# Optimization experiments

Measured on AMD Instinct MI355X. Metric: run time of the kernel, lower is better.

The kernel has to match this reference:

```python
import jax, jax.numpy as jnp
import numpy as np

B, T, D, NH, L, E, K = 2, 1024, 512, 8, 4, 8, 2
H = D * 4
HD = D // NH
EPS = 1e-5
THETA = 10000.0
MOE_LAYERS = (0, 2)   # layer_idx % moe_freq == 0
DENSE_LAYERS = (1, 3)


def setup_inputs() -> dict:
    key = jax.random.key(0)
    ks = jax.random.split(key, 12)
    s = 0.02
    return {
        "x": jax.random.normal(ks[0], (B, T, D), jnp.float32),
        "qkv_w": jax.random.normal(ks[1], (L, 3 * D, D), jnp.float32) * s,
        "out_w": jax.random.normal(ks[2], (L, D, D), jnp.float32) * s,
        "norm1_w": jnp.ones((L, D), jnp.float32),
        "norm2_w": jnp.ones((L, D), jnp.float32),
        "router_w": jax.random.normal(ks[3], (2, E, D), jnp.float32) * s,
        "moe_w1": jax.random.normal(ks[4], (2, E, H, D), jnp.float32) * s,
        "moe_w2": jax.random.normal(ks[5], (2, E, D, H), jnp.float32) * s,
        "moe_w3": jax.random.normal(ks[6], (2, E, H, D), jnp.float32) * s,
        "f_w1": jax.random.normal(ks[7], (2, H, D), jnp.float32) * s,
        "f_w2": jax.random.normal(ks[8], (2, D, H), jnp.float32) * s,
        "f_w3": jax.random.normal(ks[9], (2, H, D), jnp.float32) * s,
        "norm_f": jnp.ones((D,), jnp.float32),
    }


def rmsnorm(x, w):
    return w * x * jax.lax.rsqrt(jnp.mean(x * x, axis=-1, keepdims=True) + EPS)


def rope_tables():
    inv_freq = 1.0 / (THETA ** (jnp.arange(0, HD, 2, dtype=jnp.float32) / HD))  # [HD/2]
    t = jnp.arange(T, dtype=jnp.float32)
    freqs = t[:, None] * inv_freq[None, :]  # [T, HD/2]
    return jnp.cos(freqs), jnp.sin(freqs)


def apply_rope(x, cos, sin):  # x: [B, NH, T, HD]
    x1, x2 = jnp.split(x, 2, axis=-1)
    return jnp.concatenate([x1 * cos - x2 * sin, x1 * sin + x2 * cos], axis=-1)


def attention(x, qkv_w, out_w, cos, sin, causal):
    qkv = x @ qkv_w.T  # [B, T, 3D]
    q, k, v = jnp.split(qkv, 3, axis=-1)
    sh = lambda a: a.reshape(B, T, NH, HD).transpose(0, 2, 1, 3)  # [B, NH, T, HD]
    q, k, v = sh(q), sh(k), sh(v)
    q = apply_rope(q, cos, sin)
    k = apply_rope(k, cos, sin)
    scores = jnp.einsum('bhqd,bhkd->bhqk', q, k) / np.sqrt(HD).astype(np.float32)
    scores = jnp.where(causal, scores, jnp.finfo(scores.dtype).min)
    attn = jax.nn.softmax(scores, axis=-1)
    out = jnp.einsum('bhqk,bhkd->bhqd', attn, v)
    out = out.transpose(0, 2, 1, 3).reshape(B, T, D)
    return out @ out_w.T


def swiglu(x, w1, w2, w3):
    return (jax.nn.silu(x @ w1.T) * (x @ w3.T)) @ w2.T


def moe(x, rw, w1, w2, w3):  # x: [N, D]
    n = x.shape[0]
    logits = x @ rw.T                              # [N, E]
    top_v, top_i = jax.lax.top_k(logits, K)        # [N, K]
    wts = jax.nn.softmax(top_v, axis=-1)           # [N, K]
    # combine[t, e] = sum_i wts[t, i] * 1[top_i[t, i] == e]
    combine = jnp.zeros((n, E), x.dtype).at[jnp.arange(n)[:, None], top_i].add(wts)
    gate = jax.nn.silu(jnp.einsum('nd,ehd->neh', x, w1))
    up = jnp.einsum('nd,ehd->neh', x, w3)
    expert_out = jnp.einsum('neh,edh->ned', gate * up, w2)  # [N, E, D]
    return jnp.einsum('ne,ned->nd', combine, expert_out)


def reference(x, qkv_w, out_w, norm1_w, norm2_w, router_w, moe_w1, moe_w2,
              moe_w3, f_w1, f_w2, f_w3, norm_f):
    cos, sin = rope_tables()
    causal = jnp.tril(jnp.ones((T, T), bool))
    h = x
    for l in range(L):
        h = h + attention(rmsnorm(h, norm1_w[l]), qkv_w[l], out_w[l], cos, sin, causal)
        hn = rmsnorm(h, norm2_w[l])
        if l in MOE_LAYERS:
            m = MOE_LAYERS.index(l)
            ff = moe(hn.reshape(-1, D), router_w[m], moe_w1[m], moe_w2[m], moe_w3[m]).reshape(B, T, D)
        else:
            m = DENSE_LAYERS.index(l)
            ff = swiglu(hn, f_w1[m], f_w2[m], f_w3[m])
        h = h + ff
    return rmsnorm(h, norm_f)
```

## Files before the change

kernel.cpp:

```cpp
#include <hip/hip_runtime.h>
#include <hip/hip_bf16.h>
#include <math.h>

#define Bc 2
#define Tc 1024
#define Dc 512
#define NHc 8
#define Lc 4
#define Ec 8
#define Kc 2
#define Hc 2048
#define HDc 64
#define Nc (Bc * Tc)
#define NKc (Nc * Kc)

typedef __bf16 bf16x8 __attribute__((ext_vector_type(8)));
typedef float  f32x4  __attribute__((ext_vector_type(4)));
typedef unsigned short ushort8v __attribute__((ext_vector_type(8)));
typedef unsigned short ushort4v __attribute__((ext_vector_type(4)));

__device__ inline unsigned short f2bf(float f) {
    union { float f; unsigned u; } v; v.f = f;
    unsigned r = v.u + 0x7FFFu + ((v.u >> 16) & 1u);
    return (unsigned short)(r >> 16);
}
__device__ inline float bf2f(unsigned short b) {
    union { unsigned u; float f; } v; v.u = ((unsigned)b) << 16;
    return v.f;
}
__device__ inline void splitbf(float a, unsigned short& hi, unsigned short& lo) {
    unsigned short h = f2bf(a);
    hi = h;
    lo = f2bf(a - bf2f(h));
}
__device__ inline void split8(const float4& a, const float4& b,
                              ushort8v& h, ushort8v& l) {
    unsigned short hh, ll;
    splitbf(a.x, hh, ll); h[0] = hh; l[0] = ll;
    splitbf(a.y, hh, ll); h[1] = hh; l[1] = ll;
    splitbf(a.z, hh, ll); h[2] = hh; l[2] = ll;
    splitbf(a.w, hh, ll); h[3] = hh; l[3] = ll;
    splitbf(b.x, hh, ll); h[4] = hh; l[4] = ll;
    splitbf(b.y, hh, ll); h[5] = hh; l[5] = ll;
    splitbf(b.z, hh, ll); h[6] = hh; l[6] = ll;
    splitbf(b.w, hh, ll); h[7] = hh; l[7] = ll;
}

__global__ __launch_bounds__(256) void split_w_kernel(
    const float* __restrict__ w, unsigned short* __restrict__ hi,
    unsigned short* __restrict__ lo, int n4)
{
    int i = blockIdx.x * 256 + threadIdx.x;
    if (i >= n4) return;
    float4 v = ((const float4*)w)[i];
    ushort4v h, l;
    unsigned short a, b;
    splitbf(v.x, a, b); h[0] = a; l[0] = b;
    splitbf(v.y, a, b); h[1] = a; l[1] = b;
    splitbf(v.z, a, b); h[2] = a; l[2] = b;
    splitbf(v.w, a, b); h[3] = a; l[3] = b;
    ((ushort4v*)hi)[i] = h;
    ((ushort4v*)lo)[i] = l;
}

__global__ __launch_bounds__(256) void rmsnorm_split_kernel(
    const float* __restrict__ x, const float* __restrict__ w,
    float* __restrict__ y, unsigned short* __restrict__ yh,
    unsigned short* __restrict__ yl)
{
    int row = blockIdx.x;
    const float* xr = x + (size_t)row * Dc;
    __shared__ float red[256];
    int tid = threadIdx.x;
    float ss = 0.0f;
    for (int d = tid; d < Dc; d += 256) { float v = xr[d]; ss += v * v; }
    red[tid] = ss; __syncthreads();
    for (int s = 128; s > 0; s >>= 1) {
        if (tid < s) red[tid] += red[tid + s];
        __syncthreads();
    }
    float inv = rsqrtf(red[0] / (float)Dc + 1e-5f);
    for (int d = tid; d < Dc; d += 256) {
        float v = w[d] * xr[d] * inv;
        size_t idx = (size_t)row * Dc + d;
        y[idx] = v;
        unsigned short h, l;
        splitbf(v, h, l);
        yh[idx] = h; yl[idx] = l;
    }
}

__global__ __launch_bounds__(256) void rmsnorm_kernel(
    const float* __restrict__ x, const float* __restrict__ w,
    float* __restrict__ y)
{
    int row = blockIdx.x;
    const float* xr = x + (size_t)row * Dc;
    __shared__ float red[256];
    int tid = threadIdx.x;
    float ss = 0.0f;
    for (int d = tid; d < Dc; d += 256) { float v = xr[d]; ss += v * v; }
    red[tid] = ss; __syncthreads();
    for (int s = 128; s > 0; s >>= 1) {
        if (tid < s) red[tid] += red[tid + s];
        __syncthreads();
    }
    float inv = rsqrtf(red[0] / (float)Dc + 1e-5f);
    for (int d = tid; d < Dc; d += 256)
        y[(size_t)row * Dc + d] = w[d] * xr[d] * inv;
}

template<int MODE, int TM, int TN>
__global__ __launch_bounds__(256) void gemm3p(
    const unsigned short* __restrict__ Ahi, const unsigned short* __restrict__ Alo,
    const unsigned short* __restrict__ Whibase, const unsigned short* __restrict__ Wlobase,
    float* __restrict__ C, int M, int N, int K,
    const int* __restrict__ tok, const float* __restrict__ twt,
    const int* __restrict__ counts, const int* __restrict__ offsets,
    size_t wstride)
{
    constexpr int PAD = 40;
    constexpr int PA  = TM / 64;
    constexpr int PB  = TN / 64;
    constexpr int FM  = TM / 32;
    constexpr int FN  = TN / 32;

    int e = (MODE == 5) ? blockIdx.z : 0;
    int count = M, offs = 0;
    if (MODE == 5) {
        count = counts[e];
        offs  = offsets[e];
        if ((int)(blockIdx.y * TM) >= count) return;
    }
    const unsigned short* Whi = Whibase + (size_t)e * wstride;
    const unsigned short* Wlo = Wlobase + (size_t)e * wstride;

    __shared__ __align__(16) unsigned short Ah[TM][PAD];
    __shared__ __align__(16) unsigned short Al[TM][PAD];
    __shared__ __align__(16) unsigned short Bh[TN][PAD];
    __shared__ __align__(16) unsigned short Bl[TN][PAD];

    int tid = threadIdx.x;
    int m0 = blockIdx.y * TM, n0 = blockIdx.x * TN;
    int srow = tid >> 2;
    int scol = (tid & 3) * 8;

    int wave = tid >> 6, lane = tid & 63;
    int wm = wave >> 1, wn = wave & 1;
    int quad = lane >> 4, l16 = lane & 15;

    f32x4 acc[FM][FN];
#pragma unroll
    for (int mi = 0; mi < FM; ++mi)
#pragma unroll
        for (int ni = 0; ni < FN; ++ni)
            acc[mi][ni] = (f32x4){0.f, 0.f, 0.f, 0.f};

    size_t arow[PA];
#pragma unroll
    for (int p = 0; p < PA; ++p) {
        int row = p * 64 + srow;
        if (MODE == 5) {
            int rr = m0 + row; if (rr >= count) rr = 0;
            arow[p] = (size_t)(offs + rr) * K;
        } else {
            arow[p] = (size_t)(m0 + row) * K;
        }
    }
    size_t brow[PB];
#pragma unroll
    for (int p = 0; p < PB; ++p)
        brow[p] = (size_t)(n0 + p * 64 + srow) * K;

#define G3_LOAD(AH, AL, BH, BL, KN)                                       \
    {                                                                     \
        _Pragma("unroll")                                                 \
        for (int p = 0; p < PA; ++p) {                                    \
            AH[p] = *(const ushort8v*)(Ahi + arow[p] + (KN) + scol);      \
            AL[p] = *(const ushort8v*)(Alo + arow[p] + (KN) + scol);      \
        }                                                                 \
        _Pragma("unroll")                                                 \
        for (int p = 0; p < PB; ++p) {                                    \
            BH[p] = *(const ushort8v*)(Whi + brow[p] + (KN) + scol);      \
            BL[p] = *(const ushort8v*)(Wlo + brow[p] + (KN) + scol);      \
        }                                                                 \
    }

#define G3_STORE(AH, AL, BH, BL)                                          \
    {                                                                     \
        _Pragma("unroll")                                                 \
        for (int p = 0; p < PA; ++p) {                                    \
            *(ushort8v*)&Ah[p * 64 + srow][scol] = AH[p];                 \
            *(ushort8v*)&Al[p * 64 + srow][scol] = AL[p];                 \
        }                                                                 \
        _Pragma("unroll")                                                 \
        for (int p = 0; p < PB; ++p) {                                    \
            *(ushort8v*)&Bh[p * 64 + srow][scol] = BH[p];                 \
            *(ushort8v*)&Bl[p * 64 + srow][scol] = BL[p];                 \
        }                                                                 \
    }

#define G3_COMPUTE()                                                      \
    {                                                                     \
        bf16x8 ah[FM], al[FM], bh[FN], bl[FN];                            \
        _Pragma("unroll")                                                 \
        for (int mi = 0; mi < FM; ++mi) {                                 \
            ah[mi] = *(const bf16x8*)&Ah[wm * (TM / 2) + mi * 16 + l16][quad * 8]; \
            al[mi] = *(const bf16x8*)&Al[wm * (TM / 2) + mi * 16 + l16][quad * 8]; \
        }                                                                 \
        _Pragma("unroll")                                                 \
        for (int ni = 0; ni < FN; ++ni) {                                 \
            bh[ni] = *(const bf16x8*)&Bh[wn * (TN / 2) + ni * 16 + l16][quad * 8]; \
            bl[ni] = *(const bf16x8*)&Bl[wn * (TN / 2) + ni * 16 + l16][quad * 8]; \
        }                                                                 \
        _Pragma("unroll")                                                 \
        for (int mi = 0; mi < FM; ++mi)                                   \
            _Pragma("unroll")                                             \
            for (int ni = 0; ni < FN; ++ni) {                             \
                acc[mi][ni] = __builtin_amdgcn_mfma_f32_16x16x32_bf16(    \
                    ah[mi], bh[ni], acc[mi][ni], 0, 0, 0);                \
                acc[mi][ni] = __builtin_amdgcn_mfma_f32_16x16x32_bf16(    \
                    al[mi], bh[ni], acc[mi][ni], 0, 0, 0);                \
                acc[mi][ni] = __builtin_amdgcn_mfma_f32_16x16x32_bf16(    \
                    ah[mi], bl[ni], acc[mi][ni], 0, 0, 0);                \
            }                                                             \
    }

    ushort8v a0h[PA], a0l[PA], b0h[PB], b0l[PB];
    ushort8v a1h[PA], a1l[PA], b1h[PB], b1l[PB];
    G3_LOAD(a0h, a0l, b0h, b0l, 0)
    G3_LOAD(a1h, a1l, b1h, b1l, 32)

    for (int k0 = 0; k0 < K; k0 += 64) {
        G3_STORE(a0h, a0l, b0h, b0l)
        __syncthreads();
        if (k0 + 64 < K) G3_LOAD(a0h, a0l, b0h, b0l, k0 + 64)
        G3_COMPUTE()
        __syncthreads();
        G3_STORE(a1h, a1l, b1h, b1l)
        __syncthreads();
        if (k0 + 96 < K) G3_LOAD(a1h, a1l, b1h, b1l, k0 + 96)
        G3_COMPUTE()
        __syncthreads();
    }
#undef G3_LOAD
#undef G3_STORE
#undef G3_COMPUTE

#pragma unroll
    for (int mi = 0; mi < FM; ++mi) {
#pragma unroll
        for (int ni = 0; ni < FN; ++ni) {
            int col = n0 + wn * (TN / 2) + ni * 16 + l16;
#pragma unroll
            for (int r = 0; r < 4; ++r) {
                int row = wm * (TM / 2) + mi * 16 + quad * 4 + r;
                float v = acc[mi][ni][r];
                if (MODE == 0) {
                    C[(size_t)(m0 + row) * N + col] = v;
                } else if (MODE == 1) {
                    C[(size_t)(m0 + row) * N + col] += v;
                } else {
                    int rr = m0 + row;
                    if (rr < count) {
                        int dest = tok[offs + rr];
                        float w = twt[offs + rr];
                        atomicAdd(&C[(size_t)dest * N + col], w * v);
                    }
                }
            }
        }
    }
}

template<bool GATHER>
__global__ __launch_bounds__(256) void ffn_fusedp(
    const unsigned short* __restrict__ Ahi, const unsigned short* __restrict__ Alo,
    const unsigned short* __restrict__ W1hibase, const unsigned short* __restrict__ W1lobase,
    const unsigned short* __restrict__ W3hibase, const unsigned short* __restrict__ W3lobase,
    unsigned short* __restrict__ Thi, unsigned short* __restrict__ Tlo,
    int M, int N, int K,
    const int* __restrict__ tok, const int* __restrict__ counts,
    const int* __restrict__ offsets, size_t wstride)
{
    constexpr int TM = 64, TN = 128, PAD = 40;
    constexpr int FM = 2, FN = 4;

    int e = GATHER ? blockIdx.z : 0;
    int count = M, offs = 0;
    if (GATHER) {
        count = counts[e];
        offs  = offsets[e];
        if ((int)(blockIdx.y * TM) >= count) return;
    }
    const unsigned short* W1hi = W1hibase + (size_t)e * wstride;
    const unsigned short* W1lo = W1lobase + (size_t)e * wstride;
    const unsigned short* W3hi = W3hibase + (size_t)e * wstride;
    const unsigned short* W3lo = W3lobase + (size_t)e * wstride;

    __shared__ __align__(16) unsigned short Ah[TM][PAD];
    __shared__ __align__(16) unsigned short Al[TM][PAD];
    __shared__ __align__(16) unsigned short B1h[TN][PAD];
    __shared__ __align__(16) unsigned short B1l[TN][PAD];
    __shared__ __align__(16) unsigned short B3h[TN][PAD];
    __shared__ __align__(16) unsigned short B3l[TN][PAD];
    __shared__ int sTok[TM];

    int tid = threadIdx.x;
    int m0 = blockIdx.y * TM, n0 = blockIdx.x * TN;

    if (GATHER) {
        if (tid < TM) {
            int r = m0 + tid;
            sTok[tid] = (r < count) ? tok[offs + r] : tok[offs];
        }
        __syncthreads();
    }

    int srow = tid >> 2;
    int scol = (tid & 3) * 8;
    int wave = tid >> 6, lane = tid & 63;
    int wm = wave >> 1, wn = wave & 1;
    int quad = lane >> 4, l16 = lane & 15;

    f32x4 accg[FM][FN], accu[FM][FN];
#pragma unroll
    for (int mi = 0; mi < FM; ++mi)
#pragma unroll
        for (int ni = 0; ni < FN; ++ni) {
            accg[mi][ni] = (f32x4){0.f, 0.f, 0.f, 0.f};
            accu[mi][ni] = (f32x4){0.f, 0.f, 0.f, 0.f};
        }

    size_t arow;
    if (GATHER) arow = (size_t)sTok[srow] * K;
    else        arow = (size_t)(m0 + srow) * K;
    size_t brow[2];
    brow[0] = (size_t)(n0 + srow) * K;
    brow[1] = (size_t)(n0 + 64 + srow) * K;

    ushort8v pah, pal, p1h[2], p1l[2], p3h[2], p3l[2];
    pah = *(const ushort8v*)(Ahi + arow + scol);
    pal = *(const ushort8v*)(Alo + arow + scol);
#pragma unroll
    for (int p = 0; p < 2; ++p) {
        p1h[p] = *(const ushort8v*)(W1hi + brow[p] + scol);
        p1l[p] = *(const ushort8v*)(W1lo + brow[p] + scol);
        p3h[p] = *(const ushort8v*)(W3hi + brow[p] + scol);
        p3l[p] = *(const ushort8v*)(W3lo + brow[p] + scol);
    }

    for (int k0 = 0; k0 < K; k0 += 32) {
        *(ushort8v*)&Ah[srow][scol] = pah;
        *(ushort8v*)&Al[srow][scol] = pal;
#pragma unroll
        for (int p = 0; p < 2; ++p) {
            int row = p * 64 + srow;
            *(ushort8v*)&B1h[row][scol] = p1h[p];
            *(ushort8v*)&B1l[row][scol] = p1l[p];
            *(ushort8v*)&B3h[row][scol] = p3h[p];
            *(ushort8v*)&B3l[row][scol] = p3l[p];
        }
        __syncthreads();
        if (k0 + 32 < K) {
            int kn = k0 + 32;
            pah = *(const ushort8v*)(Ahi + arow + kn + scol);
            pal = *(const ushort8v*)(Alo + arow + kn + scol);
#pragma unroll
            for (int p = 0; p < 2; ++p) {
                p1h[p] = *(const ushort8v*)(W1hi + brow[p] + kn + scol);
                p1l[p] = *(const ushort8v*)(W1lo + brow[p] + kn + scol);
                p3h[p] = *(const ushort8v*)(W3hi + brow[p] + kn + scol);
                p3l[p] = *(const ushort8v*)(W3lo + brow[p] + kn + scol);
            }
        }

        bf16x8 ah[FM], al[FM], bh[FN], bl[FN];
#pragma unroll
        for (int mi = 0; mi < FM; ++mi) {
            ah[mi] = *(const bf16x8*)&Ah[wm * 32 + mi * 16 + l16][quad * 8];
            al[mi] = *(const bf16x8*)&Al[wm * 32 + mi * 16 + l16][quad * 8];
        }
#pragma unroll
        for (int ni = 0; ni < FN; ++ni) {
            bh[ni] = *(const bf16x8*)&B1h[wn * 64 + ni * 16 + l16][quad * 8];
            bl[ni] = *(const bf16x8*)&B1l[wn * 64 + ni * 16 + l16][quad * 8];
        }
#pragma unroll
        for (int mi = 0; mi < FM; ++mi)
#pragma unroll
            for (int ni = 0; ni < FN; ++ni) {
                accg[mi][ni] = __builtin_amdgcn_mfma_f32_16x16x32_bf16(
                    ah[mi], bh[ni], accg[mi][ni], 0, 0, 0);
                accg[mi][ni] = __builtin_amdgcn_mfma_f32_16x16x32_bf16(
                    al[mi], bh[ni], accg[mi][ni], 0, 0, 0);
                accg[mi][ni] = __builtin_amdgcn_mfma_f32_16x16x32_bf16(
                    ah[mi], bl[ni], accg[mi][ni], 0, 0, 0);
            }
#pragma unroll
        for (int ni = 0; ni < FN; ++ni) {
            bh[ni] = *(const bf16x8*)&B3h[wn * 64 + ni * 16 + l16][quad * 8];
            bl[ni] = *(const bf16x8*)&B3l[wn * 64 + ni * 16 + l16][quad * 8];
        }
#pragma unroll
        for (int mi = 0; mi < FM; ++mi)
#pragma unroll
            for (int ni = 0; ni < FN; ++ni) {
                accu[mi][ni] = __builtin_amdgcn_mfma_f32_16x16x32_bf16(
                    ah[mi], bh[ni], accu[mi][ni], 0, 0, 0);
                accu[mi][ni] = __builtin_amdgcn_mfma_f32_16x16x32_bf16(
                    al[mi], bh[ni], accu[mi][ni], 0, 0, 0);
                accu[mi][ni] = __builtin_amdgcn_mfma_f32_16x16x32_bf16(
                    ah[mi], bl[ni], accu[mi][ni], 0, 0, 0);
            }
        __syncthreads();
    }

#pragma unroll
    for (int mi = 0; mi < FM; ++mi) {
#pragma unroll
        for (int ni = 0; ni < FN; ++ni) {
            int col = n0 + wn * 64 + ni * 16 + l16;
#pragma unroll
            for (int r = 0; r < 4; ++r) {
                int row = wm * 32 + mi * 16 + quad * 4 + r;
                float g = accg[mi][ni][r];
                float u = accu[mi][ni][r];
                float t = (g / (1.0f + expf(-g))) * u;
                unsigned short th, tl;
                splitbf(t, th, tl);
                if (GATHER) {
                    int rr = m0 + row;
                    if (rr < count) {
                        size_t idx = (size_t)(offs + rr) * N + col;
                        Thi[idx] = th; Tlo[idx] = tl;
                    }
                } else {
                    size_t idx = (size_t)(m0 + row) * N + col;
                    Thi[idx] = th; Tlo[idx] = tl;
                }
            }
        }
    }
}

__global__ __launch_bounds__(256) void rope_kernel(float* __restrict__ qkv)
{
    const int HD2 = HDc / 2;
    int idx = blockIdx.x * blockDim.x + threadIdx.x;
    int total = Nc * NHc * HD2;
    if (idx >= total) return;
    int i = idx % HD2;
    int hh = (idx / HD2) % NHc;
    int n = idx / (HD2 * NHc);
    int t = n % Tc;
    float invf = expf(-(2.0f * (float)i / (float)HDc) * logf(10000.0f));
    float f = (float)t * invf;
    float c = cosf(f), s = sinf(f);
    size_t base = (size_t)n * (3 * Dc) + (size_t)hh * HDc;
    float* qp = qkv + base;
    float* kp = qkv + base + Dc;
    float q1 = qp[i], q2 = qp[i + HD2];
    qp[i]       = q1 * c - q2 * s;
    qp[i + HD2] = q1 * s + q2 * c;
    float k1 = kp[i], k2 = kp[i + HD2];
    kp[i]       = k1 * c - k2 * s;
    kp[i + HD2] = k1 * s + k2 * c;
}

__global__ __launch_bounds__(256) void attn_mfma(
    const float* __restrict__ qkv, unsigned short* __restrict__ outh,
    unsigned short* __restrict__ outl)
{
    constexpr int PAD = 72;
    __shared__ __align__(16) unsigned short Qh[64][PAD];
    __shared__ __align__(16) unsigned short Ql[64][PAD];
    __shared__ __align__(16) unsigned short Kh[64][PAD];
    __shared__ __align__(16) unsigned short Kl[64][PAD];
    __shared__ __align__(16) unsigned short Vth[64][PAD];
    __shared__ __align__(16) unsigned short Vtl[64][PAD];

    int qb = blockIdx.x, bh = blockIdx.y;
    int b = bh >> 3, hh = bh & 7;
    const int D3 = 3 * Dc;
    const float* base = qkv + (size_t)b * Tc * D3 + (size_t)hh * HDc;

    int tid = threadIdx.x;
    int wave = tid >> 6, lane = tid & 63;
    int quad = lane >> 4, l16 = lane & 15;

    int srow = tid >> 2;
    int scb  = (tid & 3) * 16;
    int vhd  = lane;
    int vkb  = wave * 16;

    {
        const float* qp = base + (size_t)(qb * 64 + srow) * D3 + scb;
        float4 q0 = *(const float4*)(qp);
        float4 q1 = *(const float4*)(qp + 4);
        float4 q2 = *(const float4*)(qp + 8);
        float4 q3 = *(const float4*)(qp + 12);
        const float sc = 0.125f;
        q0.x *= sc; q0.y *= sc; q0.z *= sc; q0.w *= sc;
        q1.x *= sc; q1.y *= sc; q1.z *= sc; q1.w *= sc;
        q2.x *= sc; q2.y *= sc; q2.z *= sc; q2.w *= sc;
        q3.x *= sc; q3.y *= sc; q3.z *= sc; q3.w *= sc;
        ushort8v h, l;
        split8(q0, q1, h, l);
        *(ushort8v*)&Qh[srow][scb]     = h;
        *(ushort8v*)&Ql[srow][scb]     = l;
        split8(q2, q3, h, l);
        *(ushort8v*)&Qh[srow][scb + 8] = h;
        *(ushort8v*)&Ql[srow][scb + 8] = l;
    }
    __syncthreads();
    bf16x8 qah[2], qal[2];
#pragma unroll
    for (int ks = 0; ks < 2; ++ks) {
        qah[ks] = *(const bf16x8*)&Qh[wave * 16 + l16][ks * 32 + quad * 8];
        qal[ks] = *(const bf16x8*)&Ql[wave * 16 + l16][ks * 32 + quad * 8];
    }

    float4 kf0, kf1, kf2, kf3;
    float vf[16];
    {
        const float* kp = base + (size_t)srow * D3 + Dc + scb;
        kf0 = *(const float4*)(kp);
        kf1 = *(const float4*)(kp + 4);
        kf2 = *(const float4*)(kp + 8);
        kf3 = *(const float4*)(kp + 12);
        const float* vp = base + (size_t)vkb * D3 + 2 * Dc + vhd;
#pragma unroll
        for (int i = 0; i < 16; ++i) vf[i] = vp[(size_t)i * D3];
    }

    f32x4 o[4];
#pragma unroll
    for (int f = 0; f < 4; ++f) o[f] = (f32x4){0.f, 0.f, 0.f, 0.f};
    float mrow[4], lrow[4];
#pragma unroll
    for (int r = 0; r < 4; ++r) { mrow[r] = -1e30f; lrow[r] = 0.0f; }

    for (int kt = 0; kt <= qb; ++kt) {
        __syncthreads();
        {
            ushort8v h, l;
            split8(kf0, kf1, h, l);
            *(ushort8v*)&Kh[srow][scb]     = h;
            *(ushort8v*)&Kl[srow][scb]     = l;
            split8(kf2, kf3, h, l);
            *(ushort8v*)&Kh[srow][scb + 8] = h;
            *(ushort8v*)&Kl[srow][scb + 8] = l;
        }
        {
            float4 v0 = make_float4(vf[0], vf[1], vf[2], vf[3]);
            float4 v1 = make_float4(vf[4], vf[5], vf[6], vf[7]);
            float4 v2 = make_float4(vf[8], vf[9], vf[10], vf[11]);
            float4 v3 = make_float4(vf[12], vf[13], vf[14], vf[15]);
            ushort8v h, l;
            split8(v0, v1, h, l);
            *(ushort8v*)&Vth[vhd][vkb]     = h;
            *(ushort8v*)&Vtl[vhd][vkb]     = l;
            split8(v2, v3, h, l);
            *(ushort8v*)&Vth[vhd][vkb + 8] = h;
            *(ushort8v*)&Vtl[vhd][vkb + 8] = l;
        }
        __syncthreads();
        if (kt < qb) {
            const float* kp = base + (size_t)((kt + 1) * 64 + srow) * D3 + Dc + scb;
            kf0 = *(const float4*)(kp);
            kf1 = *(const float4*)(kp + 4);
            kf2 = *(const float4*)(kp + 8);
            kf3 = *(const float4*)(kp + 12);
            const float* vp = base + (size_t)((kt + 1) * 64 + vkb) * D3 + 2 * Dc + vhd;
#pragma unroll
            for (int i = 0; i < 16; ++i) vf[i] = vp[(size_t)i * D3];
        }

        f32x4 s[4];
#pragma unroll
        for (int ni = 0; ni < 4; ++ni) s[ni] = (f32x4){0.f, 0.f, 0.f, 0.f};
#pragma unroll
        for (int ks = 0; ks < 2; ++ks) {
            bf16x8 kh_[4], kl_[4];
#pragma unroll
            for (int ni = 0; ni < 4; ++ni) {
                kh_[ni] = *(const bf16x8*)&Kh[ni * 16 + l16][ks * 32 + quad * 8];
                kl_[ni] = *(const bf16x8*)&Kl[ni * 16 + l16][ks * 32 + quad * 8];
            }
#pragma unroll
            for (int ni = 0; ni < 4; ++ni) {
                s[ni] = __builtin_amdgcn_mfma_f32_16x16x32_bf16(
                    qah[ks], kh_[ni], s[ni], 0, 0, 0);
                s[ni] = __builtin_amdgcn_mfma_f32_16x16x32_bf16(
                    qal[ks], kh_[ni], s[ni], 0, 0, 0);
                s[ni] = __builtin_amdgcn_mfma_f32_16x16x32_bf16(
                    qah[ks], kl_[ni], s[ni], 0, 0, 0);
            }
        }

        if (kt == qb) {
#pragma unroll
            for (int ni = 0; ni < 4; ++ni)
#pragma unroll
                for (int r = 0; r < 4; ++r)
                    if (ni * 16 + l16 > wave * 16 + quad * 4 + r)
                        s[ni][r] = -1e30f;
        }

        float al4[4];
#pragma unroll
        for (int r = 0; r < 4; ++r) {
            float rm = fmaxf(fmaxf(s[0][r], s[1][r]), fmaxf(s[2][r], s[3][r]));
            rm = fmaxf(rm, __shfl_xor(rm, 1));
            rm = fmaxf(rm, __shfl_xor(rm, 2));
            rm = fmaxf(rm, __shfl_xor(rm, 4));
            rm = fmaxf(rm, __shfl_xor(rm, 8));
            float mn = fmaxf(mrow[r], rm);
            al4[r] = __expf(mrow[r] - mn);
            mrow[r] = mn;
            float rs = 0.0f;
#pragma unroll
            for (int ni = 0; ni < 4; ++ni) {
                float pv = __expf(s[ni][r] - mn);
                s[ni][r] = pv;
                rs += pv;
            }
            rs += __shfl_xor(rs, 1);
            rs += __shfl_xor(rs, 2);
            rs += __shfl_xor(rs, 4);
            rs += __shfl_xor(rs, 8);
            lrow[r] = lrow[r] * al4[r] + rs;
        }

        __syncthreads();
#pragma unroll
        for (int ni = 0; ni < 4; ++ni)
#pragma unroll
            for (int r = 0; r < 4; ++r) {
                unsigned short hp, lp;
                splitbf(s[ni][r], hp, lp);
                Kh[wave * 16 + quad * 4 + r][ni * 16 + l16] = hp;
                Kl[wave * 16 + quad * 4 + r][ni * 16 + l16] = lp;
            }
#pragma unroll
        for (int f = 0; f < 4; ++f)
#pragma unroll
            for (int r = 0; r < 4; ++r)
                o[f][r] *= al4[r];
#pragma unroll
        for (int ks = 0; ks < 2; ++ks) {
            bf16x8 pah = *(const bf16x8*)&Kh[wave * 16 + l16][ks * 32 + quad * 8];
            bf16x8 pal = *(const bf16x8*)&Kl[wave * 16 + l16][ks * 32 + quad * 8];
#pragma unroll
            for (int f = 0; f < 4; ++f) {
                bf16x8 vh_ = *(const bf16x8*)&Vth[f * 16 + l16][ks * 32 + quad * 8];
                bf16x8 vl_ = *(const bf16x8*)&Vtl[f * 16 + l16][ks * 32 + quad * 8];
                o[f] = __builtin_amdgcn_mfma_f32_16x16x32_bf16(
                    pah, vh_, o[f], 0, 0, 0);
                o[f] = __builtin_amdgcn_mfma_f32_16x16x32_bf16(
                    pal, vh_, o[f], 0, 0, 0);
                o[f] = __builtin_amdgcn_mfma_f32_16x16x32_bf16(
                    pah, vl_, o[f], 0, 0, 0);
            }
        }
    }

#pragma unroll
    for (int r = 0; r < 4; ++r) {
        float inv = 1.0f / lrow[r];
        int q = qb * 64 + wave * 16 + quad * 4 + r;
#pragma unroll
        for (int f = 0; f < 4; ++f) {
            size_t idx = (size_t)(b * Tc + q) * Dc + hh * HDc + f * 16 + l16;
            unsigned short hp, lp;
            splitbf(o[f][r] * inv, hp, lp);
            outh[idx] = hp; outl[idx] = lp;
        }
    }
}

__global__ __launch_bounds__(64) void router_kernel(
    const float* __restrict__ x, const float* __restrict__ rw,
    float* __restrict__ logits)
{
    int n = blockIdx.x;
    int lane = threadIdx.x;
    const float* xr = x + (size_t)n * Dc;
    for (int e = 0; e < Ec; ++e) {
        const float* wr = rw + (size_t)e * Dc;
        float p = 0.0f;
        for (int d = lane; d < Dc; d += 64) p += xr[d] * wr[d];
        for (int off = 32; off > 0; off >>= 1) p += __shfl_down(p, off);
        if (lane == 0) logits[(size_t)n * Ec + e] = p;
    }
}

__global__ void zero8_kernel(int* __restrict__ counts)
{
    if (threadIdx.x < Ec) counts[threadIdx.x] = 0;
}

__global__ __launch_bounds__(256) void topk_count_kernel(
    const float* __restrict__ logits, int* __restrict__ counts,
    int2* __restrict__ eidx, float2* __restrict__ ewt)
{
    int n = blockIdx.x * blockDim.x + threadIdx.x;
    if (n >= Nc) return;
    const float* lg = logits + (size_t)n * Ec;
    int i0 = -1, i1 = -1;
    float v0 = -1e30f, v1 = -1e30f;
    for (int e = 0; e < Ec; ++e) {
        float v = lg[e];
        if (v > v0) { v1 = v0; i1 = i0; v0 = v; i0 = e; }
        else if (v > v1) { v1 = v; i1 = e; }
    }
    float e1 = expf(v1 - v0);
    float w0 = 1.0f / (1.0f + e1);
    float w1 = e1 / (1.0f + e1);
    atomicAdd(&counts[i0], 1);
    atomicAdd(&counts[i1], 1);
    eidx[n] = make_int2(i0, i1);
    ewt[n]  = make_float2(w0, w1);
}

__global__ void scan_kernel(int* __restrict__ counts, int* __restrict__ offsets)
{
    if (threadIdx.x == 0) {
        int s = 0;
        for (int e = 0; e < Ec; ++e) { offsets[e] = s; s += counts[e]; counts[e] = 0; }
    }
}

__global__ __launch_bounds__(256) void topk_place_kernel(
    const int2* __restrict__ eidx, const float2* __restrict__ ewt,
    int* __restrict__ counts, const int* __restrict__ offsets,
    int* __restrict__ tok, float* __restrict__ twt)
{
    int n = blockIdx.x * blockDim.x + threadIdx.x;
    if (n >= Nc) return;
    int2 ei = eidx[n];
    float2 w = ewt[n];
    int p0 = atomicAdd(&counts[ei.x], 1);
    int r0 = offsets[ei.x] + p0;
    tok[r0] = n; twt[r0] = w.x;
    int p1 = atomicAdd(&counts[ei.y], 1);
    int r1 = offsets[ei.y] + p1;
    tok[r1] = n; twt[r1] = w.y;
}

extern "C" void kernel_launch(void* const* d_in, const int* in_sizes, int n_in,
                              void* d_out, int out_size, void* d_ws, size_t ws_size,
                              hipStream_t stream)
{
    const float* x        = (const float*)d_in[0];
    const float* qkv_w    = (const float*)d_in[1];
    const float* out_w    = (const float*)d_in[2];
    const float* norm1_w  = (const float*)d_in[3];
    const float* norm2_w  = (const float*)d_in[4];
    const float* router_w = (const float*)d_in[5];
    const float* moe_w1   = (const float*)d_in[6];
    const float* moe_w2   = (const float*)d_in[7];
    const float* moe_w3   = (const float*)d_in[8];
    const float* f_w1     = (const float*)d_in[9];
    const float* f_w2     = (const float*)d_in[10];
    const float* f_w3     = (const float*)d_in[11];
    const float* norm_f   = (const float*)d_in[12];
    float* out = (float*)d_out;

    float* p = (float*)d_ws;
    float* h      = p;  p += Nc * Dc;
    float* xn     = p;  p += Nc * Dc;
    unsigned short* xnh = (unsigned short*)p;  p += Nc * Dc / 2;
    unsigned short* xnl = (unsigned short*)p;  p += Nc * Dc / 2;
    float* arena  = p;  p += (size_t)NKc * Hc;
    float* logits = p;  p += Nc * Ec;
    int*   counts  = (int*)p;  p += 16;
    int*   offsets = (int*)p;  p += 16;
    int2*  eidx    = (int2*)p; p += 2 * Nc;
    float* ewt     = p;        p += 2 * Nc;
    int*   tok     = (int*)p;  p += NKc;
    float* twt     = p;        p += NKc;
    unsigned short* wqh = (unsigned short*)p;
    unsigned short* wql = wqh + (size_t)3 * Dc * Dc;
    unsigned short* woh = wql + (size_t)3 * Dc * Dc;
    unsigned short* wol = woh + (size_t)Dc * Dc;
    unsigned short* wah = wol + (size_t)Dc * Dc;
    unsigned short* wal = wah + (size_t)Ec * Hc * Dc;
    unsigned short* wbh = wal + (size_t)Ec * Hc * Dc;
    unsigned short* wbl = wbh + (size_t)Ec * Hc * Dc;

    float* qkv = arena;
    unsigned short* th = (unsigned short*)arena;
    unsigned short* tl = th + (size_t)NKc * Hc;

    hipMemcpyAsync(h, x, (size_t)Nc * Dc * sizeof(float),
                   hipMemcpyDeviceToDevice, stream);

    for (int l = 0; l < Lc; ++l) {
        {
            int n4 = 3 * Dc * Dc / 4;
            split_w_kernel<<<(n4 + 255) / 256, 256, 0, stream>>>(
                qkv_w + (size_t)l * 3 * Dc * Dc, wqh, wql, n4);
        }
        rmsnorm_split_kernel<<<Nc, 256, 0, stream>>>(
            h, norm1_w + (size_t)l * Dc, xn, xnh, xnl);
        gemm3p<0, 64, 128><<<dim3(3 * Dc / 128, Nc / 64, 1), 256, 0, stream>>>(
            xnh, xnl, wqh, wql, qkv, Nc, 3 * Dc, Dc,
            nullptr, nullptr, nullptr, nullptr, 0);
        {
            int total = Nc * NHc * (HDc / 2);
            rope_kernel<<<(total + 255) / 256, 256, 0, stream>>>(qkv);
        }
        {
            int n4 = Dc * Dc / 4;
            split_w_kernel<<<(n4 + 255) / 256, 256, 0, stream>>>(
                out_w + (size_t)l * Dc * Dc, woh, wol, n4);
        }
        attn_mfma<<<dim3(Tc / 64, Bc * NHc), 256, 0, stream>>>(qkv, xnh, xnl);
        gemm3p<1, 64, 64><<<dim3(Dc / 64, Nc / 64, 1), 256, 0, stream>>>(
            xnh, xnl, woh, wol, h, Nc, Dc, Dc,
            nullptr, nullptr, nullptr, nullptr, 0);

        rmsnorm_split_kernel<<<Nc, 256, 0, stream>>>(
            h, norm2_w + (size_t)l * Dc, xn, xnh, xnl);
        if (l == 0 || l == 2) {
            int m = l / 2;
            router_kernel<<<Nc, 64, 0, stream>>>(
                xn, router_w + (size_t)m * Ec * Dc, logits);
            zero8_kernel<<<1, 64, 0, stream>>>(counts);
            topk_count_kernel<<<Nc / 256, 256, 0, stream>>>(
                logits, counts, eidx, (float2*)ewt);
            scan_kernel<<<1, 64, 0, stream>>>(counts, offsets);
            topk_place_kernel<<<Nc / 256, 256, 0, stream>>>(
                eidx, (float2*)ewt, counts, offsets, tok, twt);

            int n4 = Ec * Hc * Dc / 4;
            split_w_kernel<<<(n4 + 255) / 256, 256, 0, stream>>>(
                moe_w1 + (size_t)m * Ec * Hc * Dc, wah, wal, n4);
            split_w_kernel<<<(n4 + 255) / 256, 256, 0, stream>>>(
                moe_w3 + (size_t)m * Ec * Hc * Dc, wbh, wbl, n4);
            ffn_fusedp<true><<<dim3(Hc / 128, NKc / 64, Ec), 256, 0, stream>>>(
                xnh, xnl, wah, wal, wbh, wbl, th, tl, Nc, Hc, Dc,
                tok, counts, offsets, (size_t)Hc * Dc);
            split_w_kernel<<<(n4 + 255) / 256, 256, 0, stream>>>(
                moe_w2 + (size_t)m * Ec * Dc * Hc, wah, wal, n4);
            gemm3p<5, 64, 128><<<dim3(Dc / 128, NKc / 64, Ec), 256, 0, stream>>>(
                th, tl, wah, wal, h, Nc, Dc, Hc,
                tok, twt, counts, offsets, (size_t)Dc * Hc);
        } else {
            int m = (l - 1) / 2;
            int n4 = Hc * Dc / 4;
            split_w_kernel<<<(n4 + 255) / 256, 256, 0, stream>>>(
                f_w1 + (size_t)m * Hc * Dc, wah, wal, n4);
            split_w_kernel<<<(n4 + 255) / 256, 256, 0, stream>>>(
                f_w3 + (size_t)m * Hc * Dc, wbh, wbl, n4);
            ffn_fusedp<false><<<dim3(Hc / 128, Nc / 64, 1), 256, 0, stream>>>(
                xnh, xnl, wah, wal, wbh, wbl, th, tl, Nc, Hc, Dc,
                nullptr, nullptr, nullptr, 0);
            split_w_kernel<<<(n4 + 255) / 256, 256, 0, stream>>>(
                f_w2 + (size_t)m * Dc * Hc, wah, wal, n4);
            gemm3p<1, 64, 128><<<dim3(Dc / 128, Nc / 64, 1), 256, 0, stream>>>(
                th, tl, wah, wal, h, Nc, Dc, Hc,
                nullptr, nullptr, nullptr, nullptr, 0);
        }
    }

    rmsnorm_kernel<<<Nc, 256, 0, stream>>>(h, norm_f, out);
}
```

Baseline: 1.308 ms.

## Split-K the down and output projections, enlarge FFN gate/up tiles to 128x128

Adds a KSPLIT template parameter to gemm3p so the output projection, the dense down projection and the MoE down projection split K across grid z and accumulate into the residual with atomicAdd. This is meant to raise block counts for the narrow-N GEMMs. The fused gate/up FFN kernel moves from 64x128 tiles with 256 threads to 128x128 tiles with 512 threads, for more weight reuse per block. It also inlines the split8 helper in attention. The atomics make accumulation order nondeterministic and add memory traffic, and the larger FFN tile wastes more work on the ragged tail of each MoE expert.

```diff
diff --git a/kernel.cpp b/kernel.cpp
--- a/kernel.cpp
+++ b/kernel.cpp
@@ -33,18 +33,6 @@
     hi = h;
     lo = f2bf(a - bf2f(h));
 }
-__device__ inline void split8(const float4& a, const float4& b,
-                              ushort8v& h, ushort8v& l) {
-    unsigned short hh, ll;
-    splitbf(a.x, hh, ll); h[0] = hh; l[0] = ll;
-    splitbf(a.y, hh, ll); h[1] = hh; l[1] = ll;
-    splitbf(a.z, hh, ll); h[2] = hh; l[2] = ll;
-    splitbf(a.w, hh, ll); h[3] = hh; l[3] = ll;
-    splitbf(b.x, hh, ll); h[4] = hh; l[4] = ll;
-    splitbf(b.y, hh, ll); h[5] = hh; l[5] = ll;
-    splitbf(b.z, hh, ll); h[6] = hh; l[6] = ll;
-    splitbf(b.w, hh, ll); h[7] = hh; l[7] = ll;
-}
 
 __global__ __launch_bounds__(256) void split_w_kernel(
     const float* __restrict__ w, unsigned short* __restrict__ hi,
@@ -110,7 +98,7 @@
         y[(size_t)row * Dc + d] = w[d] * xr[d] * inv;
 }
 
-template<int MODE, int TM, int TN>
+template<int MODE, int TM, int TN, int KSPLIT>
 __global__ __launch_bounds__(256) void gemm3p(
     const unsigned short* __restrict__ Ahi, const unsigned short* __restrict__ Alo,
     const unsigned short* __restrict__ Whibase, const unsigned short* __restrict__ Wlobase,
@@ -125,7 +113,9 @@
     constexpr int FM  = TM / 32;
     constexpr int FN  = TN / 32;
 
-    int e = (MODE == 5) ? blockIdx.z : 0;
+    int zz = blockIdx.z;
+    int e  = (MODE == 5) ? zz / KSPLIT : 0;
+    int kz = (MODE == 5) ? zz % KSPLIT : zz;
     int count = M, offs = 0;
     if (MODE == 5) {
         count = counts[e];
@@ -134,6 +124,9 @@
     }
     const unsigned short* Whi = Whibase + (size_t)e * wstride;
     const unsigned short* Wlo = Wlobase + (size_t)e * wstride;
+
+    int Ksub = K / KSPLIT;
+    int kbeg = kz * Ksub;
 
     __shared__ __align__(16) unsigned short Ah[TM][PAD];
     __shared__ __align__(16) unsigned short Al[TM][PAD];
@@ -228,18 +221,18 @@
 
     ushort8v a0h[PA], a0l[PA], b0h[PB], b0l[PB];
     ushort8v a1h[PA], a1l[PA], b1h[PB], b1l[PB];
-    G3_LOAD(a0h, a0l, b0h, b0l, 0)
-    G3_LOAD(a1h, a1l, b1h, b1l, 32)
-
-    for (int k0 = 0; k0 < K; k0 += 64) {
+    G3_LOAD(a0h, a0l, b0h, b0l, kbeg)
+    G3_LOAD(a1h, a1l, b1h, b1l, kbeg + 32)
+
+    for (int k0 = kbeg; k0 < kbeg + Ksub; k0 += 64) {
         G3_STORE(a0h, a0l, b0h, b0l)
         __syncthreads();
-        if (k0 + 64 < K) G3_LOAD(a0h, a0l, b0h, b0l, k0 + 64)
+        if (k0 + 64 < kbeg + Ksub) G3_LOAD(a0h, a0l, b0h, b0l, k0 + 64)
         G3_COMPUTE()
         __syncthreads();
         G3_STORE(a1h, a1l, b1h, b1l)
         __syncthreads();
-        if (k0 + 96 < K) G3_LOAD(a1h, a1l, b1h, b1l, k0 + 96)
+        if (k0 + 96 < kbeg + Ksub) G3_LOAD(a1h, a1l, b1h, b1l, k0 + 96)
         G3_COMPUTE()
         __syncthreads();
     }
@@ -260,6 +253,8 @@
                     C[(size_t)(m0 + row) * N + col] = v;
                 } else if (MODE == 1) {
                     C[(size_t)(m0 + row) * N + col] += v;
+                } else if (MODE == 2) {
+                    atomicAdd(&C[(size_t)(m0 + row) * N + col], v);
                 } else {
                     int rr = m0 + row;
                     if (rr < count) {
@@ -274,7 +269,7 @@
 }
 
 template<bool GATHER>
-__global__ __launch_bounds__(256) void ffn_fusedp(
+__global__ __launch_bounds__(512) void ffn_fusedp(
     const unsigned short* __restrict__ Ahi, const unsigned short* __restrict__ Alo,
     const unsigned short* __restrict__ W1hibase, const unsigned short* __restrict__ W1lobase,
     const unsigned short* __restrict__ W3hibase, const unsigned short* __restrict__ W3lobase,
@@ -283,8 +278,8 @@
     const int* __restrict__ tok, const int* __restrict__ counts,
     const int* __restrict__ offsets, size_t wstride)
 {
-    constexpr int TM = 64, TN = 128, PAD = 40;
-    constexpr int FM = 2, FN = 4;
+    constexpr int TM = 128, TN = 128, PAD = 40;
+    constexpr int FM = 4, FN = 2;
 
     int e = GATHER ? blockIdx.z : 0;
     int count = M, offs = 0;
@@ -320,7 +315,7 @@
     int srow = tid >> 2;
     int scol = (tid & 3) * 8;
     int wave = tid >> 6, lane = tid & 63;
-    int wm = wave >> 1, wn = wave & 1;
+    int wm = wave >> 2, wn = wave & 3;
     int quad = lane >> 4, l16 = lane & 15;
 
     f32x4 accg[FM][FN], accu[FM][FN];
@@ -335,95 +330,89 @@
     size_t arow;
     if (GATHER) arow = (size_t)sTok[srow] * K;
     else        arow = (size_t)(m0 + srow) * K;
-    size_t brow[2];
-    brow[0] = (size_t)(n0 + srow) * K;
-    brow[1] = (size_t)(n0 + 64 + srow) * K;
-
-    ushort8v pah, pal, p1h[2], p1l[2], p3h[2], p3l[2];
+    size_t brow = (size_t)(n0 + srow) * K;
+
+    ushort8v pah, pal, p1h, p1l, p3h, p3l;
     pah = *(const ushort8v*)(Ahi + arow + scol);
     pal = *(const ushort8v*)(Alo + arow + scol);
-#pragma unroll
-    for (int p = 0; p < 2; ++p) {
-        p1h[p] = *(const ushort8v*)(W1hi + brow[p] + scol);
-        p1l[p] = *(const ushort8v*)(W1lo + brow[p] + scol);
-        p3h[p] = *(const ushort8v*)(W3hi + brow[p] + scol);
-        p3l[p] = *(const ushort8v*)(W3lo + brow[p] + scol);
-    }
+    p1h = *(const ushort8v*)(W1hi + brow + scol);
+    p1l = *(const ushort8v*)(W1lo + brow + scol);
+    p3h = *(const ushort8v*)(W3hi + brow + scol);
+    p3l = *(const ushort8v*)(W3lo + brow + scol);
 
     for (int k0 = 0; k0 < K; k0 += 32) {
-        *(ushort8v*)&Ah[srow][scol] = pah;
-        *(ushort8v*)&Al[srow][scol] = pal;
-#pragma unroll
-        for (int p = 0; p < 2; ++p) {
-            int row = p * 64 + srow;
-            *(ushort8v*)&B1h[row][scol] = p1h[p];
-            *(ushort8v*)&B1l[row][scol] = p1l[p];
-            *(ushort8v*)&B3h[row][scol] = p3h[p];
-            *(ushort8v*)&B3l[row][scol] = p3l[p];
-        }
+        *(ushort8v*)&Ah[srow][scol]  = pah;
+        *(ushort8v*)&Al[srow][scol]  = pal;
+        *(ushort8v*)&B1h[srow][scol] = p1h;
+        *(ushort8v*)&B1l[srow][scol] = p1l;
+        *(ushort8v*)&B3h[srow][scol] = p3h;
+        *(ushort8v*)&B3l[srow][scol] = p3l;
         __syncthreads();
         if (k0 + 32 < K) {
             int kn = k0 + 32;
             pah = *(const ushort8v*)(Ahi + arow + kn + scol);
             pal = *(const ushort8v*)(Alo + arow + kn + scol);
-#pragma unroll
-            for (int p = 0; p < 2; ++p) {
-                p1h[p] = *(const ushort8v*)(W1hi + brow[p] + kn + scol);
-                p1l[p] = *(const ushort8v*)(W1lo + brow[p] + kn + scol);
-                p3h[p] = *(const ushort8v*)(W3hi + brow[p] + kn + scol);
-                p3l[p] = *(const ushort8v*)(W3lo + brow[p] + kn + scol);
-            }
-        }
-
-        bf16x8 ah[FM], al[FM], bh[FN], bl[FN];
+            p1h = *(const ushort8v*)(W1hi + brow + kn + scol);
+            p1l = *(const ushort8v*)(W1lo + brow + kn + scol);
+            p3h = *(const ushort8v*)(W3hi + brow + kn + scol);
+            p3l = *(const ushort8v*)(W3lo + brow + kn + scol);
+        }
+
+        bf16x8 ah[FM], al[FM];
 #pragma unroll
         for (int mi = 0; mi < FM; ++mi) {
-            ah[mi] = *(const bf16x8*)&Ah[wm * 32 + mi * 16 + l16][quad * 8];
-            al[mi] = *(const bf16x8*)&Al[wm * 32 + mi * 16 + l16][quad * 8];
-        }
+            ah[mi] = *(const bf16x8*)&Ah[wm * 64 + mi * 16 + l16][quad * 8];
+            al[mi] = *(const bf16x8*)&Al[wm * 64 + mi * 16 + l16][quad * 8];
+        }
+        {
+            bf16x8 bh[FN], bl[FN];
+#pragma unroll
+            for (int ni = 0; ni < FN; ++ni) {
+                bh[ni] = *(const bf16x8*)&B1h[wn * 32 + ni * 16 + l16][quad * 8];
+                bl[ni] = *(const bf16x8*)&B1l[wn * 32 + ni * 16 + l16][quad * 8];
+            }
+#pragma unroll
+            for (int mi = 0; mi < FM; ++mi)
+#pragma unroll
+                for (int ni = 0; ni < FN; ++ni) {
+                    accg[mi][ni] = __builtin_amdgcn_mfma_f32_16x16x32_bf16(
+                        ah[mi], bh[ni], accg[mi][ni], 0, 0, 0);
+                    accg[mi][ni] = __builtin_amdgcn_mfma_f32_16x16x32_bf16(
+                        al[mi], bh[ni], accg[mi][ni], 0, 0, 0);
+                    accg[mi][ni] = __builtin_amdgcn_mfma_f32_16x16x32_bf16(
+                        ah[mi], bl[ni], accg[mi][ni], 0, 0, 0);
+                }
+        }
+        {
+            bf16x8 bh[FN], bl[FN];
+#pragma unroll
+            for (int ni = 0; ni < FN; ++ni) {
+                bh[ni] = *(const bf16x8*)&B3h[wn * 32 + ni * 16 + l16][quad * 8];
+                bl[ni] = *(const bf16x8*)&B3l[wn * 32 + ni * 16 + l16][quad * 8];
+            }
+#pragma unroll
+            for (int mi = 0; mi < FM; ++mi)
+#pragma unroll
+                for (int ni = 0; ni < FN; ++ni) {
+                    accu[mi][ni] = __builtin_amdgcn_mfma_f32_16x16x32_bf16(
+                        ah[mi], bh[ni], accu[mi][ni], 0, 0, 0);
+                    accu[mi][ni] = __builtin_amdgcn_mfma_f32_16x16x32_bf16(
+                        al[mi], bh[ni], accu[mi][ni], 0, 0, 0);
+                    accu[mi][ni] = __builtin_amdgcn_mfma_f32_16x16x32_bf16(
+                        ah[mi], bl[ni], accu[mi][ni], 0, 0, 0);
+                }
+        }
+        __syncthreads();
+    }
+
+#pragma unroll
+    for (int mi = 0; mi < FM; ++mi) {
 #pragma unroll
         for (int ni = 0; ni < FN; ++ni) {
-            bh[ni] = *(const bf16x8*)&B1h[wn * 64 + ni * 16 + l16][quad * 8];
-            bl[ni] = *(const bf16x8*)&B1l[wn * 64 + ni * 16 + l16][quad * 8];
-        }
-#pragma unroll
-        for (int mi = 0; mi < FM; ++mi)
-#pragma unroll
-            for (int ni = 0; ni < FN; ++ni) {
-                accg[mi][ni] = __builtin_amdgcn_mfma_f32_16x16x32_bf16(
-                    ah[mi], bh[ni], accg[mi][ni], 0, 0, 0);
-                accg[mi][ni] = __builtin_amdgcn_mfma_f32_16x16x32_bf16(
-                    al[mi], bh[ni], accg[mi][ni], 0, 0, 0);
-                accg[mi][ni] = __builtin_amdgcn_mfma_f32_16x16x32_bf16(
-                    ah[mi], bl[ni], accg[mi][ni], 0, 0, 0);
-            }
-#pragma unroll
-        for (int ni = 0; ni < FN; ++ni) {
-            bh[ni] = *(const bf16x8*)&B3h[wn * 64 + ni * 16 + l16][quad * 8];
-            bl[ni] = *(const bf16x8*)&B3l[wn * 64 + ni * 16 + l16][quad * 8];
-        }
-#pragma unroll
-        for (int mi = 0; mi < FM; ++mi)
-#pragma unroll
-            for (int ni = 0; ni < FN; ++ni) {
-                accu[mi][ni] = __builtin_amdgcn_mfma_f32_16x16x32_bf16(
-                    ah[mi], bh[ni], accu[mi][ni], 0, 0, 0);
-                accu[mi][ni] = __builtin_amdgcn_mfma_f32_16x16x32_bf16(
-                    al[mi], bh[ni], accu[mi][ni], 0, 0, 0);
-                accu[mi][ni] = __builtin_amdgcn_mfma_f32_16x16x32_bf16(
-                    ah[mi], bl[ni], accu[mi][ni], 0, 0, 0);
-            }
-        __syncthreads();
-    }
-
-#pragma unroll
-    for (int mi = 0; mi < FM; ++mi) {
-#pragma unroll
-        for (int ni = 0; ni < FN; ++ni) {
-            int col = n0 + wn * 64 + ni * 16 + l16;
+            int col = n0 + wn * 32 + ni * 16 + l16;
 #pragma unroll
             for (int r = 0; r < 4; ++r) {
-                int row = wm * 32 + mi * 16 + quad * 4 + r;
+                int row = wm * 64 + mi * 16 + quad * 4 + r;
                 float g = accg[mi][ni][r];
                 float u = accu[mi][ni][r];
                 float t = (g / (1.0f + expf(-g))) * u;
@@ -505,13 +494,28 @@
         q1.x *= sc; q1.y *= sc; q1.z *= sc; q1.w *= sc;
         q2.x *= sc; q2.y *= sc; q2.z *= sc; q2.w *= sc;
         q3.x *= sc; q3.y *= sc; q3.z *= sc; q3.w *= sc;
-        ushort8v h, l;
-        split8(q0, q1, h, l);
-        *(ushort8v*)&Qh[srow][scb]     = h;
-        *(ushort8v*)&Ql[srow][scb]     = l;
-        split8(q2, q3, h, l);
-        *(ushort8v*)&Qh[srow][scb + 8] = h;
-        *(ushort8v*)&Ql[srow][scb + 8] = l;
+        unsigned short h, l;
+        ushort8v hv, lv;
+        splitbf(q0.x, h, l); hv[0] = h; lv[0] = l;
+        splitbf(q0.y, h, l); hv[1] = h; lv[1] = l;
+        splitbf(q0.z, h, l); hv[2] = h; lv[2] = l;
+        splitbf(q0.w, h, l); hv[3] = h; lv[3] = l;
+        splitbf(q1.x, h, l); hv[4] = h; lv[4] = l;
+        splitbf(q1.y, h, l); hv[5] = h; lv[5] = l;
+        splitbf(q1.z, h, l); hv[6] = h; lv[6] = l;
+        splitbf(q1.w, h, l); hv[7] = h; lv[7] = l;
+        *(ushort8v*)&Qh[srow][scb]     = hv;
+        *(ushort8v*)&Ql[srow][scb]     = lv;
+        splitbf(q2.x, h, l); hv[0] = h; lv[0] = l;
+        splitbf(q2.y, h, l); hv[1] = h; lv[1] = l;
+        splitbf(q2.z, h, l); hv[2] = h; lv[2] = l;
+        splitbf(q2.w, h, l); hv[3] = h; lv[3] = l;
+        splitbf(q3.x, h, l); hv[4] = h; lv[4] = l;
+        splitbf(q3.y, h, l); hv[5] = h; lv[5] = l;
+        splitbf(q3.z, h, l); hv[6] = h; lv[6] = l;
+        splitbf(q3.w, h, l); hv[7] = h; lv[7] = l;
+        *(ushort8v*)&Qh[srow][scb + 8] = hv;
+        *(ushort8v*)&Ql[srow][scb + 8] = lv;
     }
     __syncthreads();
     bf16x8 qah[2], qal[2];
@@ -544,26 +548,44 @@
     for (int kt = 0; kt <= qb; ++kt) {
         __syncthreads();
         {
-            ushort8v h, l;
-            split8(kf0, kf1, h, l);
-            *(ushort8v*)&Kh[srow][scb]     = h;
-            *(ushort8v*)&Kl[srow][scb]     = l;
-            split8(kf2, kf3, h, l);
-            *(ushort8v*)&Kh[srow][scb + 8] = h;
-            *(ushort8v*)&Kl[srow][scb + 8] = l;
+            unsigned short h, l;
+            ushort8v hv, lv;
+            splitbf(kf0.x, h, l); hv[0] = h; lv[0] = l;
+            splitbf(kf0.y, h, l); hv[1] = h; lv[1] = l;
+            splitbf(kf0.z, h, l); hv[2] = h; lv[2] = l;
+            splitbf(kf0.w, h, l); hv[3] = h; lv[3] = l;
+            splitbf(kf1.x, h, l); hv[4] = h; lv[4] = l;
+            splitbf(kf1.y, h, l); hv[5] = h; lv[5] = l;
+            splitbf(kf1.z, h, l); hv[6] = h; lv[6] = l;
+            splitbf(kf1.w, h, l); hv[7] = h; lv[7] = l;
+            *(ushort8v*)&Kh[srow][scb]     = hv;
+            *(ushort8v*)&Kl[srow][scb]     = lv;
+            splitbf(kf2.x, h, l); hv[0] = h; lv[0] = l;
+            splitbf(kf2.y, h, l); hv[1] = h; lv[1] = l;
+            splitbf(kf2.z, h, l); hv[2] = h; lv[2] = l;
+            splitbf(kf2.w, h, l); hv[3] = h; lv[3] = l;
+            splitbf(kf3.x, h, l); hv[4] = h; lv[4] = l;
+            splitbf(kf3.y, h, l); hv[5] = h; lv[5] = l;
+            splitbf(kf3.z, h, l); hv[6] = h; lv[6] = l;
+            splitbf(kf3.w, h, l); hv[7] = h; lv[7] = l;
+            *(ushort8v*)&Kh[srow][scb + 8] = hv;
+            *(ushort8v*)&Kl[srow][scb + 8] = lv;
         }
         {
-            float4 v0 = make_float4(vf[0], vf[1], vf[2], vf[3]);
-            float4 v1 = make_float4(vf[4], vf[5], vf[6], vf[7]);
-            float4 v2 = make_float4(vf[8], vf[9], vf[10], vf[11]);
-            float4 v3 = make_float4(vf[12], vf[13], vf[14], vf[15]);
-            ushort8v h, l;
-            split8(v0, v1, h, l);
-            *(ushort8v*)&Vth[vhd][vkb]     = h;
-            *(ushort8v*)&Vtl[vhd][vkb]     = l;
-            split8(v2, v3, h, l);
-            *(ushort8v*)&Vth[vhd][vkb + 8] = h;
-            *(ushort8v*)&Vtl[vhd][vkb + 8] = l;
+            unsigned short h, l;
+            ushort8v hv, lv;
+#pragma unroll
+            for (int i = 0; i < 8; ++i) {
+                splitbf(vf[i], h, l); hv[i] = h; lv[i] = l;
+            }
+            *(ushort8v*)&Vth[vhd][vkb]     = hv;
+            *(ushort8v*)&Vtl[vhd][vkb]     = lv;
+#pragma unroll
+            for (int i = 0; i < 8; ++i) {
+                splitbf(vf[8 + i], h, l); hv[i] = h; lv[i] = l;
+            }
+            *(ushort8v*)&Vth[vhd][vkb + 8] = hv;
+            *(ushort8v*)&Vtl[vhd][vkb + 8] = lv;
         }
         __syncthreads();
         if (kt < qb) {
@@ -805,7 +827,7 @@
         }
         rmsnorm_split_kernel<<<Nc, 256, 0, stream>>>(
             h, norm1_w + (size_t)l * Dc, xn, xnh, xnl);
-        gemm3p<0, 64, 128><<<dim3(3 * Dc / 128, Nc / 64, 1), 256, 0, stream>>>(
+        gemm3p<0, 64, 128, 1><<<dim3(3 * Dc / 128, Nc / 64, 1), 256, 0, stream>>>(
             xnh, xnl, wqh, wql, qkv, Nc, 3 * Dc, Dc,
             nullptr, nullptr, nullptr, nullptr, 0);
         {
@@ -818,7 +840,7 @@
                 out_w + (size_t)l * Dc * Dc, woh, wol, n4);
         }
         attn_mfma<<<dim3(Tc / 64, Bc * NHc), 256, 0, stream>>>(qkv, xnh, xnl);
-        gemm3p<1, 64, 64><<<dim3(Dc / 64, Nc / 64, 1), 256, 0, stream>>>(
+        gemm3p<2, 64, 64, 2><<<dim3(Dc / 64, Nc / 64, 2), 256, 0, stream>>>(
             xnh, xnl, woh, wol, h, Nc, Dc, Dc,
             nullptr, nullptr, nullptr, nullptr, 0);
 
@@ -840,12 +862,12 @@
                 moe_w1 + (size_t)m * Ec * Hc * Dc, wah, wal, n4);
             split_w_kernel<<<(n4 + 255) / 256, 256, 0, stream>>>(
                 moe_w3 + (size_t)m * Ec * Hc * Dc, wbh, wbl, n4);
-            ffn_fusedp<true><<<dim3(Hc / 128, NKc / 64, Ec), 256, 0, stream>>>(
+            ffn_fusedp<true><<<dim3(Hc / 128, NKc / 128, Ec), 512, 0, stream>>>(
                 xnh, xnl, wah, wal, wbh, wbl, th, tl, Nc, Hc, Dc,
                 tok, counts, offsets, (size_t)Hc * Dc);
             split_w_kernel<<<(n4 + 255) / 256, 256, 0, stream>>>(
                 moe_w2 + (size_t)m * Ec * Dc * Hc, wah, wal, n4);
-            gemm3p<5, 64, 128><<<dim3(Dc / 128, NKc / 64, Ec), 256, 0, stream>>>(
+            gemm3p<5, 64, 128, 2><<<dim3(Dc / 128, NKc / 64, Ec * 2), 256, 0, stream>>>(
                 th, tl, wah, wal, h, Nc, Dc, Hc,
                 tok, twt, counts, offsets, (size_t)Dc * Hc);
         } else {
@@ -855,12 +877,12 @@
                 f_w1 + (size_t)m * Hc * Dc, wah, wal, n4);
             split_w_kernel<<<(n4 + 255) / 256, 256, 0, stream>>>(
                 f_w3 + (size_t)m * Hc * Dc, wbh, wbl, n4);
-            ffn_fusedp<false><<<dim3(Hc / 128, Nc / 64, 1), 256, 0, stream>>>(
+            ffn_fusedp<false><<<dim3(Hc / 128, Nc / 128, 1), 512, 0, stream>>>(
                 xnh, xnl, wah, wal, wbh, wbl, th, tl, Nc, Hc, Dc,
                 nullptr, nullptr, nullptr, 0);
             split_w_kernel<<<(n4 + 255) / 256, 256, 0, stream>>>(
                 f_w2 + (size_t)m * Dc * Hc, wah, wal, n4);
-            gemm3p<1, 64, 128><<<dim3(Dc / 128, Nc / 64, 1), 256, 0, stream>>>(
+            gemm3p<2, 64, 128, 2><<<dim3(Dc / 128, Nc / 64, 2), 256, 0, stream>>>(
                 th, tl, wah, wal, h, Nc, Dc, Hc,
                 nullptr, nullptr, nullptr, nullptr, 0);
         }
```

Result: faster. 1.244 ms (-4.9%).
